# Kernel optimization log

Measured on AMD Instinct MI355X. Metric: run time of the kernel, lower is better.

The kernel has to match this reference:

```python
import jax, jax.numpy as jnp
import numpy as np

BS, L, S, AMB = 64, 64, 63, 32   # batch, sentence len, opseq steps, ambiguities per step
H, E, V, MLP = 128, 300, 50000, 1024
EPS = 1e-8


def setup_inputs() -> dict:
    key = jax.random.key(0)
    ks = jax.random.split(key, 12)
    u = lambda k, shp: jax.random.uniform(k, shp, dtype=jnp.float32) * 0.1
    return {
        "sentences1": jax.random.randint(ks[0], (BS, L), 0, V, dtype=jnp.int32),
        "operations1": jax.random.randint(ks[1], (BS, S, 2 * AMB), 0, L, dtype=jnp.int32),
        "oopl1": jnp.full((BS,), L + S, dtype=jnp.int32),
        "sentences2": jax.random.randint(ks[2], (BS, L), 0, V, dtype=jnp.int32),
        "operations2": jax.random.randint(ks[3], (BS, S, 2 * AMB), 0, L, dtype=jnp.int32),
        "oopl2": jnp.full((BS,), L + S, dtype=jnp.int32),
        "W": u(ks[4], (5 * H, E)),
        "U": u(ks[5], (5 * H, 2 * H)),
        "b": jnp.zeros((5 * H,), dtype=jnp.float32),
        "energy_u": u(ks[6], (H,)),
        "unk_embedding": u(ks[7], (E,)),
        "word_embeddings": jax.random.normal(ks[8], (V, E), dtype=jnp.float32),
        "A": u(ks[9], (MLP, 4 * H)),
        "a": u(ks[10], (MLP,)),
        "inv_temperature": jnp.float32(1.0),
    }


def _gates(preact, ccL, ccR):
    # preact: [..., 5H]; tree-LSTM cell (i, fL, fR, o, u gates)
    i = jax.nn.sigmoid(preact[..., :H])
    fL = jax.nn.sigmoid(preact[..., H:2 * H])
    fR = jax.nn.sigmoid(preact[..., 2 * H:3 * H])
    o = jax.nn.sigmoid(preact[..., 3 * H:4 * H])
    u = jnp.tanh(preact[..., 4 * H:5 * H])
    c = fL * ccL + fR * ccR + i * u
    h = o * jnp.tanh(c)
    return c, h


def _run_chart(sentences, operations, W, U, b, energy_u, unk_embedding,
               word_embeddings, inv_temperature):
    bs = sentences.shape[0]
    # leaf phase: embed each word, preact = W @ emb + b, ccL = ccR = 0
    emb = jnp.where(sentences[..., None] >= 0,
                    word_embeddings[jnp.clip(sentences, 0)], unk_embedding)  # [bs,L,E]
    preact = jnp.einsum('ble,ge->blg', emb, W) + b                            # [bs,L,5H]
    c, h = _gates(preact, 0.0, 0.0)
    chart = jnp.zeros((bs, L + S, 2 * H), dtype=jnp.float32)
    chart = chart.at[:, :L, :].set(jnp.concatenate([c, h], axis=-1))

    def step(chart, inp):
        ops, pos = inp                                   # ops: [bs, 2*AMB], pos: scalar
        entries = jnp.take_along_axis(chart, ops[:, :, None].astype(jnp.int32), axis=1)
        entries = entries.reshape(bs, AMB, 2, 2 * H)     # [bs, amb, (L,R), 2H]
        ccL = entries[:, :, 0, :H]
        ccR = entries[:, :, 1, :H]
        hh = entries[:, :, :, H:].reshape(bs, AMB, 2 * H)  # concat(hL, hR)
        pre = jnp.einsum('bak,gk->bag', hh, U) + b         # [bs, amb, 5H]
        c, h = _gates(pre, ccL, ccR)
        # cosine similarity of h against energy_u
        hn = jnp.maximum(jnp.sqrt(jnp.sum(h * h, axis=-1)), EPS)
        un = jnp.maximum(jnp.sqrt(jnp.sum(energy_u * energy_u)), EPS)
        e = jnp.einsum('bah,h->ba', h, energy_u) / (hn * un)
        s = jax.nn.softmax(e * inv_temperature, axis=1)    # [bs, amb]
        combined = jnp.concatenate([jnp.einsum('ba,bah->bh', s, c),
                                    jnp.einsum('ba,bah->bh', s, h)], axis=-1)
        chart = jax.lax.dynamic_update_slice(chart, combined[:, None, :], (0, pos, 0))
        return chart, None

    ops_seq = jnp.swapaxes(operations, 0, 1)             # [S, bs, 2*AMB]
    positions = L + jnp.arange(S, dtype=jnp.int32)
    chart, _ = jax.lax.scan(step, chart, (ops_seq, positions))
    return chart


def reference(sentences1, operations1, oopl1, sentences2, operations2, oopl2,
              W, U, b, energy_u, unk_embedding, word_embeddings, A, a,
              inv_temperature):
    chart1 = _run_chart(sentences1, operations1, W, U, b, energy_u,
                        unk_embedding, word_embeddings, inv_temperature)
    chart2 = _run_chart(sentences2, operations2, W, U, b, energy_u,
                        unk_embedding, word_embeddings, inv_temperature)
    bs = chart1.shape[0]
    bidx = jnp.arange(bs)
    s1 = chart1[bidx, oopl1 - 1, H:]                     # final composed h, [bs, H]
    s2 = chart2[bidx, oopl2 - 1, H:]
    u = (s1 - s2) ** 2
    v = s1 * s2
    conc = jnp.concatenate([u, v, s1, s2], axis=1)       # [bs, 4H]
    out = jax.nn.relu(jnp.einsum('jk,ik->ij', A, conc) + a)
    return out
```

## Files before the change

### kernel.cpp

```cpp
#include <hip/hip_runtime.h>
#include <hip/hip_bf16.h>

#define BSZ 64
#define LL  64
#define SS  63
#define AMB 32
#define HH  128
#define EE  300
#define MLPN 1024
#define GG  640
#define K2  256
#define PP  127
#define CROW 272

typedef __attribute__((ext_vector_type(8))) short short8;
typedef __attribute__((ext_vector_type(4))) float f32x4;

__device__ __forceinline__ float sigf(float x) { return 1.f / (1.f + __expf(-x)); }

__device__ __forceinline__ unsigned short f2bf(float x) {
    unsigned int u = __float_as_uint(x);
    u += 0x7fffu + ((u >> 16) & 1u);
    return (unsigned short)(u >> 16);
}
__device__ __forceinline__ float bf2f(short x) {
    return __uint_as_float(((unsigned)(unsigned short)x) << 16);
}

__device__ __forceinline__ short8 cvt8(f32x4 x0, f32x4 x1) {
    short8 v;
    v[0]=(short)f2bf(x0[0]); v[1]=(short)f2bf(x0[1]);
    v[2]=(short)f2bf(x0[2]); v[3]=(short)f2bf(x0[3]);
    v[4]=(short)f2bf(x1[0]); v[5]=(short)f2bf(x1[1]);
    v[6]=(short)f2bf(x1[2]); v[7]=(short)f2bf(x1[3]);
    return v;
}

__global__ void __launch_bounds__(1024, 4) leaf_kernel(
        const int* __restrict__ sent1, const int* __restrict__ sent2,
        const float* __restrict__ W, const float* __restrict__ bias,
        const float* __restrict__ unk, const float* __restrict__ wemb,
        short* __restrict__ chartG) {
    __shared__ __align__(16) short AsL[2 * 10 * 64 * 8];
    const int tid = threadIdx.x;
    const int blk = blockIdx.x, pair = blk >> 1, half = blk & 1;
    const int ch = pair >> 6, b = pair & 63;
    const int* sent = ch ? sent2 : sent1;
    const int w = tid >> 6, lane = tid & 63, quad = lane >> 4, l15 = lane & 15;

    {
        float ef[2][8];
        int est[2], eso[2];
#pragma unroll
        for (int i = 0; i < 2; ++i) {
            int slot = i * 1024 + tid;
            est[i] = -1;
            if (slot < 1280) {
                int tloc = slot / 40, oct = slot - tloc * 40;
                est[i] = tloc; eso[i] = oct;
                int sid = sent[b * LL + half * 32 + tloc];
                const float* src = (sid >= 0) ? (wemb + (size_t)sid * EE) : unk;
                int k0 = oct * 8;
                if (k0 + 8 <= EE) {
                    f32x4 x0 = *(const f32x4*)(src + k0);
                    f32x4 x1 = *(const f32x4*)(src + k0 + 4);
                    ef[i][0]=x0[0]; ef[i][1]=x0[1]; ef[i][2]=x0[2]; ef[i][3]=x0[3];
                    ef[i][4]=x1[0]; ef[i][5]=x1[1]; ef[i][6]=x1[2]; ef[i][7]=x1[3];
                } else {
#pragma unroll
                    for (int j = 0; j < 8; ++j) ef[i][j] = (k0 + j < EE) ? src[k0 + j] : 0.f;
                }
            }
        }
#pragma unroll
        for (int i = 0; i < 2; ++i) {
            if (est[i] >= 0) {
                int tloc = est[i], oct = eso[i];
                short8 v;
#pragma unroll
                for (int j = 0; j < 8; ++j) v[j] = (short)f2bf(ef[i][j]);
                *(short8*)(AsL + (((tloc >> 4) * 10 + (oct >> 2)) * 64
                                  + ((oct & 3) << 4) + (tloc & 15)) * 8) = v;
            }
        }
    }
    __syncthreads();

    const int mt2 = w & 1, nu = w >> 1;
    const int koff = quad << 3;
    const float* Wr0 = W + (size_t)(nu * 16 + l15) * EE;
    const float* Wr1 = W + (size_t)((nu + 24) * 16 + l15) * EE;
    const float* Wr2 = W + (size_t)((nu + 32) * 16 + l15) * EE;
    f32x4 acc[3] = {};
#pragma unroll 2
    for (int kk = 0; kk < 10; ++kk) {
        short8 a0 = *(const short8*)(AsL + ((mt2 * 10 + kk) * 64 + lane) * 8);
        int k0 = kk * 32 + koff;
        short8 b0, b1, b2;
        if (k0 + 8 <= EE) {
            b0 = cvt8(*(const f32x4*)(Wr0 + k0), *(const f32x4*)(Wr0 + k0 + 4));
            b1 = cvt8(*(const f32x4*)(Wr1 + k0), *(const f32x4*)(Wr1 + k0 + 4));
            b2 = cvt8(*(const f32x4*)(Wr2 + k0), *(const f32x4*)(Wr2 + k0 + 4));
        } else {
#pragma unroll
            for (int j = 0; j < 8; ++j) {
                float f0 = 0.f, f1 = 0.f, f2 = 0.f;
                if (k0 + j < EE) { f0 = Wr0[k0 + j]; f1 = Wr1[k0 + j]; f2 = Wr2[k0 + j]; }
                b0[j] = (short)f2bf(f0); b1[j] = (short)f2bf(f1); b2[j] = (short)f2bf(f2);
            }
        }
        acc[0] = __builtin_amdgcn_mfma_f32_16x16x32_bf16(a0, b0, acc[0], 0, 0, 0);
        acc[1] = __builtin_amdgcn_mfma_f32_16x16x32_bf16(a0, b1, acc[1], 0, 0, 0);
        acc[2] = __builtin_amdgcn_mfma_f32_16x16x32_bf16(a0, b2, acc[2], 0, 0, 0);
    }

    {
        int jc = nu * 16 + l15;
        float bi = bias[jc], bo = bias[3 * HH + jc], bu = bias[4 * HH + jc];
        size_t pb = (size_t)pair * 16384;
#pragma unroll
        for (int r = 0; r < 4; ++r) {
            float cv = sigf(acc[0][r] + bi) * tanhf(acc[2][r] + bu);
            float hv = sigf(acc[1][r] + bo) * tanhf(cv);
            int l = half * 32 + mt2 * 16 + quad * 4 + r;
            chartG[pb + (size_t)l * 256 + jc]      = (short)f2bf(cv);
            chartG[pb + (size_t)l * 256 + HH + jc] = (short)f2bf(hv);
        }
    }
}

__global__ void __launch_bounds__(1024, 4) step_kernel(
        const int* __restrict__ ops1, const int* __restrict__ ops2,
        const int* __restrict__ oopl1, const int* __restrict__ oopl2,
        const float* __restrict__ U, const float* __restrict__ bias,
        const float* __restrict__ eu, const float* __restrict__ invt,
        const short* __restrict__ chartG, float* __restrict__ fin) {
    __shared__ __align__(16) short chartL[127 * CROW + 16];
    __shared__ __align__(16) short As2[2 * 8 * 64 * 8];
    __shared__ __align__(16) float chh[32 * 132];
    __shared__ __align__(16) int ops_all[SS * 64];
    __shared__ unsigned long long smask[64];
    __shared__ int live_list[SS];
    __shared__ float e_num[AMB], h2s[AMB], s_w[AMB];
    __shared__ float comb[2][2][HH];
    __shared__ int nl_sh;
    __shared__ float un_sh;

    const int tid = threadIdx.x;
    const int pair = blockIdx.x, ch = pair >> 6, b = pair & 63;
    const int* ops  = ch ? ops2 : ops1;
    const int* oopl = ch ? oopl2 : oopl1;
    const float it = invt[0];
    const int w = tid >> 6, lane = tid & 63, quad = lane >> 4, l15 = lane & 15;

    const int4* cg = (const int4*)(chartG + (size_t)pair * 16384);
    int4 c0 = cg[tid];
    int4 c1 = cg[1024 + tid];
    int4 opv = make_int4(0, 0, 0, 0);
    if (tid < 1008) opv = ((const int4*)(ops + (size_t)b * SS * 64))[tid];
    if (tid < 64) {
        float v = eu[tid] * eu[tid] + eu[tid + 64] * eu[tid + 64];
        for (int off = 32; off >= 1; off >>= 1) v += __shfl_xor(v, off);
        if (tid == 0) un_sh = fmaxf(sqrtf(v), 1e-8f);
    }
#pragma unroll
    for (int i = 0; i < 3; ++i) {
        int idx = i * 1024 + tid;
        if (idx < 2142)
            ((int4*)(chartL + 64 * CROW))[idx] = make_int4(0, 0, 0, 0);
    }
    {
        int r0 = tid >> 5, cq0 = tid & 31;
        *(int4*)(chartL + r0 * CROW + (cq0 << 3)) = c0;
        int t2 = 1024 + tid;
        int r1 = t2 >> 5, cq1 = t2 & 31;
        *(int4*)(chartL + r1 * CROW + (cq1 << 3)) = c1;
    }
    {
        opv.x = min(max(opv.x, 0), PP - 1);
        opv.y = min(max(opv.y, 0), PP - 1);
        opv.z = min(max(opv.z, 0), PP - 1);
        opv.w = min(max(opv.w, 0), PP - 1);
        if (tid < 1008) ((int4*)ops_all)[tid] = opv;

        int t = tid >> 4;
        unsigned long long bit = 0ull;
        if (tid < 1008) {
            int q;
            q = opv.x - LL; if (q >= 0 && q < t) bit |= 1ull << q;
            q = opv.y - LL; if (q >= 0 && q < t) bit |= 1ull << q;
            q = opv.z - LL; if (q >= 0 && q < t) bit |= 1ull << q;
            q = opv.w - LL; if (q >= 0 && q < t) bit |= 1ull << q;
        }
        bit |= __shfl_xor(bit, 1);
        bit |= __shfl_xor(bit, 2);
        bit |= __shfl_xor(bit, 4);
        bit |= __shfl_xor(bit, 8);
        if ((lane & 15) == 0 && t < SS) smask[t] = bit;
    }
    __syncthreads();

    if (w == 0) {
        unsigned long long my = (lane < SS) ? smask[lane] : 0ull;
        unsigned long long m = 0ull;
        int q0 = oopl[b] - 1 - LL;
        if (q0 >= 0) { if (q0 > SS - 1) q0 = SS - 1; m = 1ull << q0; }
        while (true) {
            unsigned long long c = ((m >> lane) & 1ull) ? my : 0ull;
            for (int off = 32; off >= 1; off >>= 1) c |= __shfl_xor(c, off);
            unsigned long long nm = m | c;
            if (nm == m) break;
            m = nm;
        }
        if (lane == 0) {
            int n = 0;
            for (int t = 0; t < SS; ++t)
                if ((m >> t) & 1) live_list[n++] = t;
            nl_sh = n;
        }
    }
    __syncthreads();

    const int nl = nl_sh;
    const float eul = eu[lane], euh = eu[64 + lane];
    const int smt = w & 1, snu = w >> 1;
    const int sjc = snu * 16 + l15;
    const float bi  = bias[sjc],          bfl = bias[HH + sjc];
    const float bfr = bias[2 * HH + sjc], bo  = bias[3 * HH + sjc];
    const float bu  = bias[4 * HH + sjc];
    const int ukoff = quad << 3;
    const float* Ur0 = U + (size_t)((snu +  0) * 16 + l15) * K2;
    const float* Ur1 = U + (size_t)((snu +  8) * 16 + l15) * K2;
    const float* Ur2 = U + (size_t)((snu + 16) * 16 + l15) * K2;
    const float* Ur3 = U + (size_t)((snu + 24) * 16 + l15) * K2;
    const float* Ur4 = U + (size_t)((snu + 32) * 16 + l15) * K2;

    for (int sidx = 0; sidx < nl; ++sidx) {
        const int t = live_list[sidx];
        const int* oprow = ops_all + t * 64;

        {
            int a = tid >> 5, oct = tid & 31, side = oct >> 4, m8 = oct & 15;
            int row = oprow[2 * a + side];
            short8 v = *(const short8*)(chartL + row * CROW + HH + m8 * 8);
            *(short8*)(As2 + (((a >> 4) * 8 + (oct >> 2)) * 64
                              + ((oct & 3) << 4) + (a & 15)) * 8) = v;
        }
        __syncthreads();

        float cvals[4], hvals[4];
        {
            f32x4 acc[5] = {};
#pragma unroll 2
            for (int kk = 0; kk < 8; ++kk) {
                short8 a0 = *(const short8*)(As2 + ((smt * 8 + kk) * 64 + lane) * 8);
                int k0 = kk * 32 + ukoff;
                short8 b0 = cvt8(*(const f32x4*)(Ur0 + k0), *(const f32x4*)(Ur0 + k0 + 4));
                short8 b1 = cvt8(*(const f32x4*)(Ur1 + k0), *(const f32x4*)(Ur1 + k0 + 4));
                short8 b2 = cvt8(*(const f32x4*)(Ur2 + k0), *(const f32x4*)(Ur2 + k0 + 4));
                short8 b3 = cvt8(*(const f32x4*)(Ur3 + k0), *(const f32x4*)(Ur3 + k0 + 4));
                short8 b4 = cvt8(*(const f32x4*)(Ur4 + k0), *(const f32x4*)(Ur4 + k0 + 4));
                acc[0] = __builtin_amdgcn_mfma_f32_16x16x32_bf16(a0, b0, acc[0], 0, 0, 0);
                acc[1] = __builtin_amdgcn_mfma_f32_16x16x32_bf16(a0, b1, acc[1], 0, 0, 0);
                acc[2] = __builtin_amdgcn_mfma_f32_16x16x32_bf16(a0, b2, acc[2], 0, 0, 0);
                acc[3] = __builtin_amdgcn_mfma_f32_16x16x32_bf16(a0, b3, acc[3], 0, 0, 0);
                acc[4] = __builtin_amdgcn_mfma_f32_16x16x32_bf16(a0, b4, acc[4], 0, 0, 0);
            }
#pragma unroll
            for (int r = 0; r < 4; ++r) {
                int a = smt * 16 + quad * 4 + r;
                float ccLv = bf2f(chartL[oprow[2 * a] * CROW + sjc]);
                float ccRv = bf2f(chartL[oprow[2 * a + 1] * CROW + sjc]);
                float cv = sigf(acc[1][r] + bfl) * ccLv
                         + sigf(acc[2][r] + bfr) * ccRv
                         + sigf(acc[0][r] + bi) * tanhf(acc[4][r] + bu);
                float hv = sigf(acc[3][r] + bo) * tanhf(cv);
                cvals[r] = cv; hvals[r] = hv;
                chh[a * 132 + sjc] = hv;
            }
        }
        __syncthreads();

#pragma unroll
        for (int i = 0; i < 2; ++i) {
            int a = w * 2 + i;
            float h0 = chh[a * 132 + lane], h1 = chh[a * 132 + 64 + lane];
            float pe = h0 * eul + h1 * euh;
            float pn = h0 * h0 + h1 * h1;
            for (int off = 32; off >= 1; off >>= 1) {
                pe += __shfl_xor(pe, off);
                pn += __shfl_xor(pn, off);
            }
            if (lane == 0) { e_num[a] = pe; h2s[a] = pn; }
        }
        __syncthreads();

        if (tid < 64) {
            float v = (tid < AMB)
                ? (e_num[tid] / (fmaxf(sqrtf(h2s[tid]), 1e-8f) * un_sh)) * it
                : -3.4e38f;
            float m = v;
            for (int off = 32; off >= 1; off >>= 1) m = fmaxf(m, __shfl_xor(m, off));
            float ex = (tid < AMB) ? __expf(v - m) : 0.f;
            float su = ex;
            for (int off = 32; off >= 1; off >>= 1) su += __shfl_xor(su, off);
            if (tid < AMB) s_w[tid] = ex / su;
        }
        __syncthreads();

        {
            float sc = 0.f, sh = 0.f;
#pragma unroll
            for (int r = 0; r < 4; ++r) {
                int a = smt * 16 + quad * 4 + r;
                float sw = s_w[a];
                sc = fmaf(sw, cvals[r], sc);
                sh = fmaf(sw, hvals[r], sh);
            }
            sc += __shfl_xor(sc, 16); sc += __shfl_xor(sc, 32);
            sh += __shfl_xor(sh, 16); sh += __shfl_xor(sh, 32);
            if (lane < 16) {
                comb[smt][0][sjc] = sc;
                comb[smt][1][sjc] = sh;
            }
        }
        __syncthreads();
        if (tid < K2) {
            int part = tid >> 7, col = tid & 127;
            float val = comb[0][part][col] + comb[1][part][col];
            chartL[(LL + t) * CROW + part * HH + col] = (short)f2bf(val);
        }
        __syncthreads();
    }

    int p = min(max(oopl[b] - 1, 0), PP - 1);
    if (tid < K2)
        fin[(size_t)pair * K2 + tid] = bf2f(chartL[p * CROW + tid]);
}

__global__ void __launch_bounds__(256) mlp_kernel(
        const float* __restrict__ fin,
        const float* __restrict__ A, const float* __restrict__ abias,
        float* __restrict__ out) {
    __shared__ __align__(16) float conc[4][512];
    const int tid = threadIdx.x;
    const int jt = blockIdx.x & 15, bt = blockIdx.x >> 4;

#pragma unroll
    for (int i = 0; i < 2; ++i) {
        int s = i * 256 + tid;
        int bl = s >> 7, kv = s & 127;
        int k0 = kv * 4, sel = k0 >> 7, kk0 = k0 & 127;
        int b = bt * 4 + bl;
        f32x4 s1 = *(const f32x4*)(fin + (size_t)b * K2 + HH + kk0);
        f32x4 s2 = *(const f32x4*)(fin + (size_t)(BSZ + b) * K2 + HH + kk0);
        f32x4 v;
        if (sel == 0)      { f32x4 d = s1 - s2; v = d * d; }
        else if (sel == 1) v = s1 * s2;
        else if (sel == 2) v = s1;
        else               v = s2;
        *(f32x4*)&conc[bl][k0] = v;
    }
    __syncthreads();

    const int jj = tid & 63, bg = tid >> 6;
    const int j = jt * 64 + jj, b = bt * 4 + bg;
    const float* Arow = A + (size_t)j * 512;
    float acc0 = abias[j], acc1 = 0.f;
    for (int k = 0; k < 512; k += 8) {
        f32x4 a0 = *(const f32x4*)(Arow + k);
        f32x4 a1 = *(const f32x4*)(Arow + k + 4);
        f32x4 c0 = *(const f32x4*)&conc[bg][k];
        f32x4 c1 = *(const f32x4*)&conc[bg][k + 4];
#pragma unroll
        for (int u = 0; u < 4; ++u) {
            acc0 = fmaf(a0[u], c0[u], acc0);
            acc1 = fmaf(a1[u], c1[u], acc1);
        }
    }
    out[(size_t)b * MLPN + j] = fmaxf(acc0 + acc1, 0.f);
}

extern "C" void kernel_launch(void* const* d_in, const int* in_sizes, int n_in,
                              void* d_out, int out_size, void* d_ws, size_t ws_size,
                              hipStream_t stream) {
    const int*   sent1 = (const int*)d_in[0];
    const int*   ops1  = (const int*)d_in[1];
    const int*   oopl1 = (const int*)d_in[2];
    const int*   sent2 = (const int*)d_in[3];
    const int*   ops2  = (const int*)d_in[4];
    const int*   oopl2 = (const int*)d_in[5];
    const float* W     = (const float*)d_in[6];
    const float* U     = (const float*)d_in[7];
    const float* bias  = (const float*)d_in[8];
    const float* eu    = (const float*)d_in[9];
    const float* unk   = (const float*)d_in[10];
    const float* wemb  = (const float*)d_in[11];
    const float* A     = (const float*)d_in[12];
    const float* ab    = (const float*)d_in[13];
    const float* invt  = (const float*)d_in[14];
    float* out = (float*)d_out;
    (void)in_sizes; (void)n_in; (void)out_size; (void)ws_size;

    char* ws = (char*)d_ws;
    const size_t CHG_OFF = 0;
    const size_t FIN_OFF = 4194304;
    short* chartG = (short*)(ws + CHG_OFF);
    float* fin    = (float*)(ws + FIN_OFF);

    leaf_kernel<<<256, 1024, 0, stream>>>(sent1, sent2, W, bias, unk, wemb, chartG);

    step_kernel<<<128, 1024, 0, stream>>>(ops1, ops2, oopl1, oopl2,
                                          U, bias, eu, invt, chartG, fin);

    mlp_kernel<<<256, 256, 0, stream>>>(fin, A, ab, out);
}
```

Before: 199.2 us.

## Pre-convert W and U to bf16 MFMA-fragment layout in a prep kernel

Adds a prep kernel that converts W and U once per call to bf16 and stores them in the exact per-lane fragment order the MFMA loops consume. The leaf and step kernels then load one contiguous short8 per fragment instead of two strided fp32 vectors plus an in-loop conversion. This matters most in the step loop, which reran the fp32-to-bf16 conversion of U on every live step. The leaf loop is also software-pipelined with double-buffered B fragments. The cost is an extra kernel launch and workspace traffic, and the leaf kernel's launch bounds drop the min-blocks hint.

```diff
diff --git a/kernel.cpp b/kernel.cpp
--- a/kernel.cpp
+++ b/kernel.cpp
@@ -36,9 +36,40 @@
     return v;
 }
 
-__global__ void __launch_bounds__(1024, 4) leaf_kernel(
+#define PWT 25600
+#define PUT 20480
+__global__ void __launch_bounds__(256) prep_kernel(
+        const float* __restrict__ W, const float* __restrict__ U,
+        short* __restrict__ WTB, short* __restrict__ UTB) {
+    int idx = blockIdx.x * 256 + threadIdx.x;
+    if (idx < PWT) {
+        int g = idx / 40, cc = idx - g * 40;
+        int k0 = cc * 8;
+        float f[8];
+#pragma unroll
+        for (int j = 0; j < 8; ++j)
+            f[j] = (k0 + j < EE) ? W[(size_t)g * EE + k0 + j] : 0.f;
+        short8 v;
+#pragma unroll
+        for (int j = 0; j < 8; ++j) v[j] = (short)f2bf(f[j]);
+        int n = g >> 4, l15 = g & 15;
+        int kk = k0 >> 5, quad = (k0 >> 3) & 3;
+        *(short8*)(WTB + ((size_t)((n * 10 + kk) * 64 + quad * 16 + l15)) * 8) = v;
+    } else if (idx < PWT + PUT) {
+        int o = idx - PWT;
+        int g = o >> 5, cc = o & 31;
+        int k0 = cc * 8;
+        f32x4 x0 = *(const f32x4*)(U + (size_t)g * K2 + k0);
+        f32x4 x1 = *(const f32x4*)(U + (size_t)g * K2 + k0 + 4);
+        int n = g >> 4, l15 = g & 15;
+        int kk = k0 >> 5, quad = (k0 >> 3) & 3;
+        *(short8*)(UTB + ((size_t)((n * 8 + kk) * 64 + quad * 16 + l15)) * 8) = cvt8(x0, x1);
+    }
+}
+
+__global__ void __launch_bounds__(1024) leaf_kernel(
         const int* __restrict__ sent1, const int* __restrict__ sent2,
-        const float* __restrict__ W, const float* __restrict__ bias,
+        const short* __restrict__ WTB, const float* __restrict__ bias,
         const float* __restrict__ unk, const float* __restrict__ wemb,
         short* __restrict__ chartG) {
     __shared__ __align__(16) short AsL[2 * 10 * 64 * 8];
@@ -87,32 +118,28 @@
     __syncthreads();
 
     const int mt2 = w & 1, nu = w >> 1;
-    const int koff = quad << 3;
-    const float* Wr0 = W + (size_t)(nu * 16 + l15) * EE;
-    const float* Wr1 = W + (size_t)((nu + 24) * 16 + l15) * EE;
-    const float* Wr2 = W + (size_t)((nu + 32) * 16 + l15) * EE;
     f32x4 acc[3] = {};
-#pragma unroll 2
-    for (int kk = 0; kk < 10; ++kk) {
+    short8 bb0[3], bb1[3];
+#define LDW(dst, kkv) do { \
+    dst[0] = *(const short8*)(WTB + ((size_t)((nu +  0) * 10 + (kkv)) * 64 + lane) * 8); \
+    dst[1] = *(const short8*)(WTB + ((size_t)((nu + 24) * 10 + (kkv)) * 64 + lane) * 8); \
+    dst[2] = *(const short8*)(WTB + ((size_t)((nu + 32) * 10 + (kkv)) * 64 + lane) * 8); \
+} while (0)
+    LDW(bb0, 0);
+#pragma unroll 1
+    for (int kk = 0; kk < 10; kk += 2) {
+        LDW(bb1, kk + 1);
         short8 a0 = *(const short8*)(AsL + ((mt2 * 10 + kk) * 64 + lane) * 8);
-        int k0 = kk * 32 + koff;
-        short8 b0, b1, b2;
-        if (k0 + 8 <= EE) {
-            b0 = cvt8(*(const f32x4*)(Wr0 + k0), *(const f32x4*)(Wr0 + k0 + 4));
-            b1 = cvt8(*(const f32x4*)(Wr1 + k0), *(const f32x4*)(Wr1 + k0 + 4));
-            b2 = cvt8(*(const f32x4*)(Wr2 + k0), *(const f32x4*)(Wr2 + k0 + 4));
-        } else {
-#pragma unroll
-            for (int j = 0; j < 8; ++j) {
-                float f0 = 0.f, f1 = 0.f, f2 = 0.f;
-                if (k0 + j < EE) { f0 = Wr0[k0 + j]; f1 = Wr1[k0 + j]; f2 = Wr2[k0 + j]; }
-                b0[j] = (short)f2bf(f0); b1[j] = (short)f2bf(f1); b2[j] = (short)f2bf(f2);
-            }
-        }
-        acc[0] = __builtin_amdgcn_mfma_f32_16x16x32_bf16(a0, b0, acc[0], 0, 0, 0);
-        acc[1] = __builtin_amdgcn_mfma_f32_16x16x32_bf16(a0, b1, acc[1], 0, 0, 0);
-        acc[2] = __builtin_amdgcn_mfma_f32_16x16x32_bf16(a0, b2, acc[2], 0, 0, 0);
-    }
+        acc[0] = __builtin_amdgcn_mfma_f32_16x16x32_bf16(a0, bb0[0], acc[0], 0, 0, 0);
+        acc[1] = __builtin_amdgcn_mfma_f32_16x16x32_bf16(a0, bb0[1], acc[1], 0, 0, 0);
+        acc[2] = __builtin_amdgcn_mfma_f32_16x16x32_bf16(a0, bb0[2], acc[2], 0, 0, 0);
+        if (kk + 2 < 10) LDW(bb0, kk + 2);
+        short8 a1 = *(const short8*)(AsL + ((mt2 * 10 + kk + 1) * 64 + lane) * 8);
+        acc[0] = __builtin_amdgcn_mfma_f32_16x16x32_bf16(a1, bb1[0], acc[0], 0, 0, 0);
+        acc[1] = __builtin_amdgcn_mfma_f32_16x16x32_bf16(a1, bb1[1], acc[1], 0, 0, 0);
+        acc[2] = __builtin_amdgcn_mfma_f32_16x16x32_bf16(a1, bb1[2], acc[2], 0, 0, 0);
+    }
+#undef LDW
 
     {
         int jc = nu * 16 + l15;
@@ -132,7 +159,7 @@
 __global__ void __launch_bounds__(1024, 4) step_kernel(
         const int* __restrict__ ops1, const int* __restrict__ ops2,
         const int* __restrict__ oopl1, const int* __restrict__ oopl2,
-        const float* __restrict__ U, const float* __restrict__ bias,
+        const short* __restrict__ UTB, const float* __restrict__ bias,
         const float* __restrict__ eu, const float* __restrict__ invt,
         const short* __restrict__ chartG, float* __restrict__ fin) {
     __shared__ __align__(16) short chartL[127 * CROW + 16];
@@ -228,12 +255,6 @@
     const float bi  = bias[sjc],          bfl = bias[HH + sjc];
     const float bfr = bias[2 * HH + sjc], bo  = bias[3 * HH + sjc];
     const float bu  = bias[4 * HH + sjc];
-    const int ukoff = quad << 3;
-    const float* Ur0 = U + (size_t)((snu +  0) * 16 + l15) * K2;
-    const float* Ur1 = U + (size_t)((snu +  8) * 16 + l15) * K2;
-    const float* Ur2 = U + (size_t)((snu + 16) * 16 + l15) * K2;
-    const float* Ur3 = U + (size_t)((snu + 24) * 16 + l15) * K2;
-    const float* Ur4 = U + (size_t)((snu + 32) * 16 + l15) * K2;
 
     for (int sidx = 0; sidx < nl; ++sidx) {
         const int t = live_list[sidx];
@@ -251,20 +272,13 @@
         float cvals[4], hvals[4];
         {
             f32x4 acc[5] = {};
-#pragma unroll 2
             for (int kk = 0; kk < 8; ++kk) {
                 short8 a0 = *(const short8*)(As2 + ((smt * 8 + kk) * 64 + lane) * 8);
-                int k0 = kk * 32 + ukoff;
-                short8 b0 = cvt8(*(const f32x4*)(Ur0 + k0), *(const f32x4*)(Ur0 + k0 + 4));
-                short8 b1 = cvt8(*(const f32x4*)(Ur1 + k0), *(const f32x4*)(Ur1 + k0 + 4));
-                short8 b2 = cvt8(*(const f32x4*)(Ur2 + k0), *(const f32x4*)(Ur2 + k0 + 4));
-                short8 b3 = cvt8(*(const f32x4*)(Ur3 + k0), *(const f32x4*)(Ur3 + k0 + 4));
-                short8 b4 = cvt8(*(const f32x4*)(Ur4 + k0), *(const f32x4*)(Ur4 + k0 + 4));
-                acc[0] = __builtin_amdgcn_mfma_f32_16x16x32_bf16(a0, b0, acc[0], 0, 0, 0);
-                acc[1] = __builtin_amdgcn_mfma_f32_16x16x32_bf16(a0, b1, acc[1], 0, 0, 0);
-                acc[2] = __builtin_amdgcn_mfma_f32_16x16x32_bf16(a0, b2, acc[2], 0, 0, 0);
-                acc[3] = __builtin_amdgcn_mfma_f32_16x16x32_bf16(a0, b3, acc[3], 0, 0, 0);
-                acc[4] = __builtin_amdgcn_mfma_f32_16x16x32_bf16(a0, b4, acc[4], 0, 0, 0);
+#pragma unroll
+                for (int s5 = 0; s5 < 5; ++s5) {
+                    short8 bv = *(const short8*)(UTB + ((size_t)((snu + 8 * s5) * 8 + kk) * 64 + lane) * 8);
+                    acc[s5] = __builtin_amdgcn_mfma_f32_16x16x32_bf16(a0, bv, acc[s5], 0, 0, 0);
+                }
             }
 #pragma unroll
             for (int r = 0; r < 4; ++r) {
@@ -403,15 +417,21 @@
     (void)in_sizes; (void)n_in; (void)out_size; (void)ws_size;
 
     char* ws = (char*)d_ws;
-    const size_t CHG_OFF = 0;
-    const size_t FIN_OFF = 4194304;
+    const size_t WTB_OFF = 0;
+    const size_t UTB_OFF = 409600;
+    const size_t CHG_OFF = 737280;
+    const size_t FIN_OFF = 4931584;
+    short* WTB    = (short*)(ws + WTB_OFF);
+    short* UTB    = (short*)(ws + UTB_OFF);
     short* chartG = (short*)(ws + CHG_OFF);
     float* fin    = (float*)(ws + FIN_OFF);
 
-    leaf_kernel<<<256, 1024, 0, stream>>>(sent1, sent2, W, bias, unk, wemb, chartG);
+    prep_kernel<<<180, 256, 0, stream>>>(W, U, WTB, UTB);
+
+    leaf_kernel<<<256, 1024, 0, stream>>>(sent1, sent2, WTB, bias, unk, wemb, chartG);
 
     step_kernel<<<128, 1024, 0, stream>>>(ops1, ops2, oopl1, oopl2,
-                                          U, bias, eu, invt, chartG, fin);
+                                          UTB, bias, eu, invt, chartG, fin);
 
     mlp_kernel<<<256, 256, 0, stream>>>(fin, A, ab, out);
 }
```

After: 183.6 us (median of 2 runs). -7.8%, faster.
